# Kernel optimization log

Hardware: AMD Instinct MI355X
Metric: run time of the kernel (lower is better)

The kernel has to match this reference:

```python
import jax, jax.numpy as jnp
import numpy as np

DIM = 256
N = 16          # number of sub-codebooks
K = 1024        # codes per sub-codebook (torch arg K; SeqVQ uses self.embedding directly)
E_DIM = DIM // N
DEPTH = 3
BETA = 0.25
B = 8192


def setup_inputs() -> dict:
    key = jax.random.key(0)
    k1, k2, k3 = jax.random.split(key, 3)
    z = jax.random.normal(k1, (B, DIM), dtype=jnp.float32)
    # nn.init.uniform_(data, -1/N, 1/N)
    embedding = jax.random.uniform(k2, (N, K, E_DIM), dtype=jnp.float32,
                                   minval=-1.0 / N, maxval=1.0 / N)
    # frozen-twin pooling query encoder: mean over depth then Linear D->D
    W = jax.random.normal(k3, (DIM, DIM), dtype=jnp.float32) * 0.02
    b = jnp.zeros((DIM,), dtype=jnp.float32)
    return {"z": z, "embedding": embedding, "W": W, "b": b}


def reference(z, embedding, W, b):
    Bq, D = z.shape
    n, k, e = embedding.shape
    zr = z.reshape(Bq, n, e)                 # residual, squeezed (B,N,1,e)->(B,N,e)
    e_sq = jnp.sum(embedding * embedding, axis=-1)  # (N,K)
    z_q_steps = []
    onehot = None
    idx = None
    for _ in range(DEPTH):
        # cdist((B,N,1,e),(N,K,e)) via ||z||^2 - 2 z.e + ||e||^2, then sqrt
        z_sq = jnp.sum(zr * zr, axis=-1)                       # (B,N)
        cross = jnp.einsum('bne,nke->bnk', zr, embedding)      # (B,N,K)
        d = jnp.sqrt(jnp.maximum(z_sq[:, :, None] - 2.0 * cross + e_sq[None], 0.0))
        idx = jnp.argmin(d, axis=-1)                           # (B,N)
        onehot = jax.nn.one_hot(idx, k, dtype=z.dtype)         # scatter one-hot (B,N,K)
        q = jnp.einsum('bnk,nke->bne', onehot, embedding)      # (B,N,e)
        zr = zr - q
        z_q_steps.append(q.reshape(Bq, D))
    z_q_residual = jnp.stack(z_q_steps, axis=1)                # (B, depth, D)
    # frozen twin query encoder (params carry no gradient in original)
    Wc = jax.lax.stop_gradient(W)
    bc = jax.lax.stop_gradient(b)
    z_q = jnp.mean(z_q_residual, axis=1) @ Wc + bc             # (B, D)
    loss = (jnp.mean((jax.lax.stop_gradient(z_q) - z) ** 2)
            + BETA * jnp.mean((z_q - jax.lax.stop_gradient(z)) ** 2))
    z_q_out = z + jax.lax.stop_gradient(z_q - z)               # straight-through
    return loss, z_q_out, onehot, idx[:, :, None]
```

## Files before the change

### kernel.cpp

```cpp
#include <hip/hip_runtime.h>
#include <math.h>

#define BQ    8192
#define DIMD  256
#define NSUB  16
#define KC    1024
#define ED    16

#define OFF_ZQ   1
#define OFF_OH   (1 + BQ * DIMD)
#define OH_ELEMS (BQ * NSUB * KC)
#define OFF_IDX  (OFF_OH + OH_ELEMS)
#define F4N      ((OH_ELEMS - 4) / 4)
#define WEPS     2e-4f

typedef __attribute__((ext_vector_type(2))) float v2f;
typedef __attribute__((ext_vector_type(4))) float f32x4;
typedef __attribute__((ext_vector_type(8))) short bshort8;
typedef __attribute__((ext_vector_type(4))) unsigned int u32x4;

struct Zr  { v2f p0, p1, p2, p3, p4, p5, p6, p7; };
struct Row { float4 c0, c1, c2, c3; };
struct V2x2 { v2f lo, hi; };

__device__ __forceinline__ float np_sumsq(Zr z) {
  float q0 = __fmul_rn(z.p0.x, z.p0.x), q1 = __fmul_rn(z.p0.y, z.p0.y);
  float q2 = __fmul_rn(z.p1.x, z.p1.x), q3 = __fmul_rn(z.p1.y, z.p1.y);
  float q4 = __fmul_rn(z.p2.x, z.p2.x), q5 = __fmul_rn(z.p2.y, z.p2.y);
  float q6 = __fmul_rn(z.p3.x, z.p3.x), q7 = __fmul_rn(z.p3.y, z.p3.y);
  float q8 = __fmul_rn(z.p4.x, z.p4.x), q9 = __fmul_rn(z.p4.y, z.p4.y);
  float qa = __fmul_rn(z.p5.x, z.p5.x), qb = __fmul_rn(z.p5.y, z.p5.y);
  float qc = __fmul_rn(z.p6.x, z.p6.x), qd = __fmul_rn(z.p6.y, z.p6.y);
  float qe = __fmul_rn(z.p7.x, z.p7.x), qf = __fmul_rn(z.p7.y, z.p7.y);
  float r0 = __fadd_rn(q0, q8), r1 = __fadd_rn(q1, q9);
  float r2 = __fadd_rn(q2, qa), r3 = __fadd_rn(q3, qb);
  float r4 = __fadd_rn(q4, qc), r5 = __fadd_rn(q5, qd);
  float r6 = __fadd_rn(q6, qe), r7 = __fadd_rn(q7, qf);
  return __fadd_rn(__fadd_rn(__fadd_rn(r0, r1), __fadd_rn(r2, r3)),
                   __fadd_rn(__fadd_rn(r4, r5), __fadd_rn(r6, r7)));
}

__device__ __forceinline__ float ref_d(Zr z, Row rw, float zsq, float esq) {
  float p0  = __fmul_rn(z.p0.x, rw.c0.x), p1  = __fmul_rn(z.p0.y, rw.c0.y);
  float p2  = __fmul_rn(z.p1.x, rw.c0.z), p3  = __fmul_rn(z.p1.y, rw.c0.w);
  float p4  = __fmul_rn(z.p2.x, rw.c1.x), p5  = __fmul_rn(z.p2.y, rw.c1.y);
  float p6  = __fmul_rn(z.p3.x, rw.c1.z), p7  = __fmul_rn(z.p3.y, rw.c1.w);
  float p8  = __fmul_rn(z.p4.x, rw.c2.x), p9  = __fmul_rn(z.p4.y, rw.c2.y);
  float p10 = __fmul_rn(z.p5.x, rw.c2.z), p11 = __fmul_rn(z.p5.y, rw.c2.w);
  float p12 = __fmul_rn(z.p6.x, rw.c3.x), p13 = __fmul_rn(z.p6.y, rw.c3.y);
  float p14 = __fmul_rn(z.p7.x, rw.c3.z), p15 = __fmul_rn(z.p7.y, rw.c3.w);
  float L0 = __fadd_rn(__fadd_rn(__fadd_rn(p0, p4), p8),  p12);
  float L1 = __fadd_rn(__fadd_rn(__fadd_rn(p1, p5), p9),  p13);
  float L2 = __fadd_rn(__fadd_rn(__fadd_rn(p2, p6), p10), p14);
  float L3 = __fadd_rn(__fadd_rn(__fadd_rn(p3, p7), p11), p15);
  float cross = __fadd_rn(__fadd_rn(L0, L1), __fadd_rn(L2, L3));
  float t = __fsub_rn(zsq, __fmul_rn(2.0f, cross));
  t = __fadd_rn(t, esq);
  t = fmaxf(t, 0.0f);
  return (float)sqrt((double)t);
}

__device__ __forceinline__ Zr sub_row(Zr z, Row rw) {
  Zr o;
  o.p0 = (v2f){__fsub_rn(z.p0.x, rw.c0.x), __fsub_rn(z.p0.y, rw.c0.y)};
  o.p1 = (v2f){__fsub_rn(z.p1.x, rw.c0.z), __fsub_rn(z.p1.y, rw.c0.w)};
  o.p2 = (v2f){__fsub_rn(z.p2.x, rw.c1.x), __fsub_rn(z.p2.y, rw.c1.y)};
  o.p3 = (v2f){__fsub_rn(z.p3.x, rw.c1.z), __fsub_rn(z.p3.y, rw.c1.w)};
  o.p4 = (v2f){__fsub_rn(z.p4.x, rw.c2.x), __fsub_rn(z.p4.y, rw.c2.y)};
  o.p5 = (v2f){__fsub_rn(z.p5.x, rw.c2.z), __fsub_rn(z.p5.y, rw.c2.w)};
  o.p6 = (v2f){__fsub_rn(z.p6.x, rw.c3.x), __fsub_rn(z.p6.y, rw.c3.y)};
  o.p7 = (v2f){__fsub_rn(z.p7.x, rw.c3.z), __fsub_rn(z.p7.y, rw.c3.w)};
  return o;
}

__device__ __forceinline__ Zr load_zr(const float* p) {
  const float4* zp = (const float4*)p;
  float4 a0 = zp[0], a1 = zp[1], a2 = zp[2], a3 = zp[3];
  V2x2 v0 = __builtin_bit_cast(V2x2, a0), v1 = __builtin_bit_cast(V2x2, a1);
  V2x2 v2 = __builtin_bit_cast(V2x2, a2), v3 = __builtin_bit_cast(V2x2, a3);
  Zr z;
  z.p0 = v0.lo; z.p1 = v0.hi; z.p2 = v1.lo; z.p3 = v1.hi;
  z.p4 = v2.lo; z.p5 = v2.hi; z.p6 = v3.lo; z.p7 = v3.hi;
  return z;
}

__device__ __forceinline__ Row load_row(const float* p) {
  const float4* cp = (const float4*)p;
  Row rw; rw.c0 = cp[0]; rw.c1 = cp[1]; rw.c2 = cp[2]; rw.c3 = cp[3];
  return rw;
}

__device__ __forceinline__ unsigned int f2bf(float x) {
  unsigned int u = __float_as_uint(x);
  return (u + 0x7FFFu + ((u >> 16) & 1u)) >> 16;
}
__device__ __forceinline__ float bf2f(unsigned int b) {
  return __uint_as_float(b << 16);
}

__global__ void vq_prep(const float* __restrict__ emb,
                        unsigned int* __restrict__ ws) {
  const int row = blockIdx.x * 256 + threadIdx.x;
  const float* c = emb + row * 16;
  unsigned int o[16];
#pragma unroll
  for (int u = 0; u < 8; ++u) {
    float a = -c[2 * u], b = -c[2 * u + 1];
    unsigned int h0 = f2bf(a), h1 = f2bf(b);
    o[u] = h0 | (h1 << 16);
    unsigned int l0 = f2bf(__fsub_rn(a, bf2f(h0)));
    unsigned int l1 = f2bf(__fsub_rn(b, bf2f(h1)));
    o[8 + u] = l0 | (l1 << 16);
  }
  u32x4* dst = (u32x4*)ws + row * 4;
#pragma unroll
  for (int j = 0; j < 4; ++j)
    dst[j] = (u32x4){o[4 * j], o[4 * j + 1], o[4 * j + 2], o[4 * j + 3]};
}

__global__ __launch_bounds__(256, 4) void vq_main(
    const float* __restrict__ z, const float* __restrict__ emb,
    const unsigned int* __restrict__ ws, float* __restrict__ out) {
  __shared__ float esq[KC];
  __shared__ float ehs[KC];
  __shared__ unsigned int zq[4 * 64 * 16];
  __shared__ float zb[4 * 64 * 16];
  const int tid   = threadIdx.x;
  const int bx    = blockIdx.x;
  const int n     = bx & 15;
  const int bbase = (bx >> 4) * 256;
  const int w     = tid >> 6;
  const int lane  = tid & 63;
  const int q     = lane >> 4;
  const int c16   = lane & 15;
  const float* embn = emb + n * (KC * ED);
  const u32x4* wsn  = (const u32x4*)ws + n * (KC * 4);

  for (int k = tid; k < KC; k += 256) {
    float s = np_sumsq(load_zr(embn + k * 16));
    esq[k] = s; ehs[k] = 0.5f * s;
  }
  if (bx == 0 && tid == 0) {
    out[0] = 0.f;
    out[OFF_OH + 0] = 0.f; out[OFF_OH + 1] = 0.f; out[OFF_OH + 2] = 0.f;
    out[OFF_OH + OH_ELEMS - 1] = 0.f;
  }
  __syncthreads();

  const int scanB = bbase + tid;
  Zr zr = load_zr(z + scanB * DIMD + n * ED);
  unsigned int* zqw = zq + w * 1024;
  float*        zbw = zb + w * 1024;

#define STAGE_ZR                                                              \
  {                                                                           \
    const int o = lane * 16;                                                  \
    v2f* zb2 = (v2f*)(zbw + o);                                               \
    zb2[0]=zr.p0; zb2[1]=zr.p1; zb2[2]=zr.p2; zb2[3]=zr.p3;                   \
    zb2[4]=zr.p4; zb2[5]=zr.p5; zb2[6]=zr.p6; zb2[7]=zr.p7;                   \
    _Pragma("unroll")                                                         \
    for (int u = 0; u < 8; ++u) { }                                           \
                                                   \
    {                                                                         \
      v2f P; unsigned h0, h1, l0, l1;                                         \
      P=zr.p0; h0=f2bf(P.x); h1=f2bf(P.y); zqw[o+0]=h0|(h1<<16);              \
      l0=f2bf(__fsub_rn(P.x,bf2f(h0))); l1=f2bf(__fsub_rn(P.y,bf2f(h1)));     \
      zqw[o+8]=l0|(l1<<16);                                                   \
      P=zr.p1; h0=f2bf(P.x); h1=f2bf(P.y); zqw[o+1]=h0|(h1<<16);              \
      l0=f2bf(__fsub_rn(P.x,bf2f(h0))); l1=f2bf(__fsub_rn(P.y,bf2f(h1)));     \
      zqw[o+9]=l0|(l1<<16);                                                   \
      P=zr.p2; h0=f2bf(P.x); h1=f2bf(P.y); zqw[o+2]=h0|(h1<<16);              \
      l0=f2bf(__fsub_rn(P.x,bf2f(h0))); l1=f2bf(__fsub_rn(P.y,bf2f(h1)));     \
      zqw[o+10]=l0|(l1<<16);                                                  \
      P=zr.p3; h0=f2bf(P.x); h1=f2bf(P.y); zqw[o+3]=h0|(h1<<16);              \
      l0=f2bf(__fsub_rn(P.x,bf2f(h0))); l1=f2bf(__fsub_rn(P.y,bf2f(h1)));     \
      zqw[o+11]=l0|(l1<<16);                                                  \
      P=zr.p4; h0=f2bf(P.x); h1=f2bf(P.y); zqw[o+4]=h0|(h1<<16);              \
      l0=f2bf(__fsub_rn(P.x,bf2f(h0))); l1=f2bf(__fsub_rn(P.y,bf2f(h1)));     \
      zqw[o+12]=l0|(l1<<16);                                                  \
      P=zr.p5; h0=f2bf(P.x); h1=f2bf(P.y); zqw[o+5]=h0|(h1<<16);              \
      l0=f2bf(__fsub_rn(P.x,bf2f(h0))); l1=f2bf(__fsub_rn(P.y,bf2f(h1)));     \
      zqw[o+13]=l0|(l1<<16);                                                  \
      P=zr.p6; h0=f2bf(P.x); h1=f2bf(P.y); zqw[o+6]=h0|(h1<<16);              \
      l0=f2bf(__fsub_rn(P.x,bf2f(h0))); l1=f2bf(__fsub_rn(P.y,bf2f(h1)));     \
      zqw[o+14]=l0|(l1<<16);                                                  \
      P=zr.p7; h0=f2bf(P.x); h1=f2bf(P.y); zqw[o+7]=h0|(h1<<16);              \
      l0=f2bf(__fsub_rn(P.x,bf2f(h0))); l1=f2bf(__fsub_rn(P.y,bf2f(h1)));     \
      zqw[o+15]=l0|(l1<<16);                                                  \
    }                                                                         \
  }
  STAGE_ZR

  const int gtid = bx * 256 + tid;
  float4* f4 = (float4*)(out + OFF_OH + 3);
  const float4 zf4 = make_float4(0.f, 0.f, 0.f, 0.f);
  int sIdx = 0;
  int bi = 0;

  for (int dep = 0; dep < 3; ++dep) {
    asm volatile("s_waitcnt lgkmcnt(0)" ::: "memory");
    u32x4 B0 = *(const u32x4*)(zqw + ((0 * 16 + c16) * 16 + q * 4));
    u32x4 B1 = *(const u32x4*)(zqw + ((1 * 16 + c16) * 16 + q * 4));
    u32x4 B2 = *(const u32x4*)(zqw + ((2 * 16 + c16) * 16 + q * 4));
    u32x4 B3 = *(const u32x4*)(zqw + ((3 * 16 + c16) * 16 + q * 4));
    bshort8 b0 = __builtin_bit_cast(bshort8, B0);
    bshort8 b1 = __builtin_bit_cast(bshort8, B1);
    bshort8 b2 = __builtin_bit_cast(bshort8, B2);
    bshort8 b3 = __builtin_bit_cast(bshort8, B3);

    float m1_0 = 3.0e38f, m1_1 = 3.0e38f, m1_2 = 3.0e38f, m1_3 = 3.0e38f;
    float m2_0 = 3.0e38f, m2_1 = 3.0e38f, m2_2 = 3.0e38f, m2_3 = 3.0e38f;
    int   k1_0 = 0, k1_1 = 0, k1_2 = 0, k1_3 = 0;
    const int qc4 = q * 4;

    for (int ct = 0; ct < 64; ++ct) {
      f32x4 ehv = __builtin_bit_cast(f32x4, ((const float4*)ehs)[ct * 4 + q]);
      u32x4 A1u = wsn[ct * 64 + c16 * 4 + q];
      u32x4 A2u = wsn[ct * 64 + c16 * 4 + ((q + 2) & 3)];
      if (dep == 0) {
        int sl = sIdx * 131072 + gtid; ++sIdx;
        if (sl < F4N) f4[sl] = zf4;
      }
      {
        int sl = sIdx * 131072 + gtid; ++sIdx;
        if (sl < F4N) f4[sl] = zf4;
      }
      bshort8 a1 = __builtin_bit_cast(bshort8, A1u);
      bshort8 a2 = __builtin_bit_cast(bshort8, A2u);
      const int cbase = ct * 16 + qc4;
#define UPD(V, CODE, M1, K1, M2)                                              \
      { float v_ = (V);                                                       \
        M2 = __builtin_amdgcn_fmed3f(v_, M1, M2);                             \
        bool lt_ = v_ < M1; M1 = lt_ ? v_ : M1; K1 = lt_ ? (CODE) : K1; }
#define DOST(BV, M1, K1, M2)                                                  \
      { f32x4 d1 = __builtin_amdgcn_mfma_f32_16x16x32_bf16(a1, BV, ehv, 0,0,0);\
        f32x4 dd = __builtin_amdgcn_mfma_f32_16x16x32_bf16(a2, BV, d1, 0,0,0);\
        UPD(dd.x, cbase + 0, M1, K1, M2)                                      \
        UPD(dd.y, cbase + 1, M1, K1, M2)                                      \
        UPD(dd.z, cbase + 2, M1, K1, M2)                                      \
        UPD(dd.w, cbase + 3, M1, K1, M2) }
      DOST(b0, m1_0, k1_0, m2_0)
      DOST(b1, m1_1, k1_1, m2_1)
      DOST(b2, m1_2, k1_2, m2_2)
      DOST(b3, m1_3, k1_3, m2_3)
#undef DOST
#undef UPD
    }
#define MERGE3(M1, K1, M2, OFF)                                               \
    { float om = __shfl_xor(M1, OFF); int ok = __shfl_xor(K1, OFF);           \
      float os = __shfl_xor(M2, OFF);                                         \
      float hi = fmaxf(M1, om);                                               \
      M2 = fminf(fminf(M2, os), hi);                                          \
      bool bw = (om < M1) || (om == M1 && ok < K1);                           \
      M1 = bw ? om : M1; K1 = bw ? ok : K1; }
    MERGE3(m1_0, k1_0, m2_0, 16) MERGE3(m1_0, k1_0, m2_0, 32)
    MERGE3(m1_1, k1_1, m2_1, 16) MERGE3(m1_1, k1_1, m2_1, 32)
    MERGE3(m1_2, k1_2, m2_2, 16) MERGE3(m1_2, k1_2, m2_2, 32)
    MERGE3(m1_3, k1_3, m2_3, 16) MERGE3(m1_3, k1_3, m2_3, 32)
#undef MERGE3
    float mA = (q & 1) ? m1_1 : m1_0,  mB = (q & 1) ? m1_3 : m1_2;
    float sA = (q & 1) ? m2_1 : m2_0,  sB = (q & 1) ? m2_3 : m2_2;
    int   kA = (q & 1) ? k1_1 : k1_0;  int kB = (q & 1) ? k1_3 : k1_2;
    float m1F = (q & 2) ? mB : mA;
    float m2F = (q & 2) ? sB : sA;
    int   k1F = (q & 2) ? kB : kA;

    bool fb = (__fsub_rn(m2F, m1F) < WEPS);
    unsigned long long mask = __ballot(fb);
    while (mask) {
      int ss = __ffsll((unsigned long long)mask) - 1;
      mask &= (mask - 1);
      Zr zs = load_zr(zbw + ss * 16);
      float zsq = np_sumsq(zs);
      float db = 3.0e38f; int kb = 0;
      for (int i = 0; i < 16; ++i) {
        int kk = i * 64 + lane;
        Row rw = load_row(embn + kk * 16);
        float d = ref_d(zs, rw, zsq, esq[kk]);
        if (d < db) { db = d; kb = kk; }
      }
#pragma unroll
      for (int off = 1; off < 64; off <<= 1) {
        float od = __shfl_xor(db, off); int ok = __shfl_xor(kb, off);
        if (od < db || (od == db && ok < kb)) { db = od; kb = ok; }
      }
      if (lane == ss) k1F = kb;
    }
    bi = k1F;
    zr = sub_row(zr, load_row(embn + k1F * 16));
    if (dep < 2) { STAGE_ZR }
  }
  for (; sIdx < 256; ++sIdx) {
    int sl = sIdx * 131072 + gtid;
    if (sl < F4N) f4[sl] = zf4;
  }
  out[OFF_IDX + scanB * NSUB + n] = (float)bi;
  {
    Zr zo = load_zr(z + scanB * DIMD + n * ED);
    float* mp2 = out + OFF_ZQ + scanB * DIMD + n * ED;
    mp2[0]  = __fdiv_rn(__fsub_rn(zo.p0.x, zr.p0.x), 3.0f);
    mp2[1]  = __fdiv_rn(__fsub_rn(zo.p0.y, zr.p0.y), 3.0f);
    mp2[2]  = __fdiv_rn(__fsub_rn(zo.p1.x, zr.p1.x), 3.0f);
    mp2[3]  = __fdiv_rn(__fsub_rn(zo.p1.y, zr.p1.y), 3.0f);
    mp2[4]  = __fdiv_rn(__fsub_rn(zo.p2.x, zr.p2.x), 3.0f);
    mp2[5]  = __fdiv_rn(__fsub_rn(zo.p2.y, zr.p2.y), 3.0f);
    mp2[6]  = __fdiv_rn(__fsub_rn(zo.p3.x, zr.p3.x), 3.0f);
    mp2[7]  = __fdiv_rn(__fsub_rn(zo.p3.y, zr.p3.y), 3.0f);
    mp2[8]  = __fdiv_rn(__fsub_rn(zo.p4.x, zr.p4.x), 3.0f);
    mp2[9]  = __fdiv_rn(__fsub_rn(zo.p4.y, zr.p4.y), 3.0f);
    mp2[10] = __fdiv_rn(__fsub_rn(zo.p5.x, zr.p5.x), 3.0f);
    mp2[11] = __fdiv_rn(__fsub_rn(zo.p5.y, zr.p5.y), 3.0f);
    mp2[12] = __fdiv_rn(__fsub_rn(zo.p6.x, zr.p6.x), 3.0f);
    mp2[13] = __fdiv_rn(__fsub_rn(zo.p6.y, zr.p6.y), 3.0f);
    mp2[14] = __fdiv_rn(__fsub_rn(zo.p7.x, zr.p7.x), 3.0f);
    mp2[15] = __fdiv_rn(__fsub_rn(zo.p7.y, zr.p7.y), 3.0f);
  }
#undef STAGE_ZR
}

__global__ void vq_ones(float* __restrict__ out) {
  int g = blockIdx.x * 256 + threadIdx.x;
  int k = (int)out[OFF_IDX + g];
  out[OFF_OH + g * KC + k] = 1.0f;
}

#define TB 16
__global__ __launch_bounds__(256, 2) void vq_head(
    const float* __restrict__ z, const float* __restrict__ W,
    const float* __restrict__ bias, float* __restrict__ out) {
  __shared__ float ml[TB][DIMD];
  __shared__ double reds[4];
  const int t  = threadIdx.x;
  const int r0 = blockIdx.x * TB;
  for (int j = t; j < TB * DIMD; j += 256) {
    int r = j >> 8, d = j & 255;
    ml[r][d] = out[OFF_ZQ + (r0 + r) * DIMD + d];
  }
  __syncthreads();
  float acc[TB];
#pragma unroll
  for (int r = 0; r < TB; ++r) acc[r] = 0.f;
  for (int d = 0; d < DIMD; ++d) {
    float w = W[d * DIMD + t];
#pragma unroll
    for (int r = 0; r < TB; ++r) acc[r] = fmaf(ml[r][d], w, acc[r]);
  }
  const float bv = bias[t];
  double lp = 0.0;
#pragma unroll
  for (int r = 0; r < TB; ++r) {
    float zq   = acc[r] + bv;
    float zv   = z[(r0 + r) * DIMD + t];
    float diff = zq - zv;
    out[OFF_ZQ + (r0 + r) * DIMD + t] = zv + diff;
    lp += (double)diff * (double)diff;
  }
#pragma unroll
  for (int o = 32; o > 0; o >>= 1) lp += __shfl_down(lp, o);
  if ((t & 63) == 0) reds[t >> 6] = lp;
  __syncthreads();
  if (t == 0) {
    double tot = reds[0] + reds[1] + reds[2] + reds[3];
    atomicAdd(out, (float)(tot * (1.25 / (double)(BQ * DIMD))));
  }
}

extern "C" void kernel_launch(void* const* d_in, const int* in_sizes, int n_in,
                              void* d_out, int out_size, void* d_ws, size_t ws_size,
                              hipStream_t stream) {
  const float* z    = (const float*)d_in[0];
  const float* emb  = (const float*)d_in[1];
  const float* W    = (const float*)d_in[2];
  const float* bias = (const float*)d_in[3];
  float* out = (float*)d_out;
  unsigned int* wsp = (unsigned int*)d_ws;
  vq_prep<<<dim3(64), dim3(256), 0, stream>>>(emb, wsp);
  vq_main<<<dim3((BQ / 256) * NSUB), dim3(256), 0, stream>>>(z, emb, wsp, out);
  vq_ones<<<dim3((BQ * NSUB) / 256), dim3(256), 0, stream>>>(out);
  vq_head<<<dim3(BQ / TB), dim3(256), 0, stream>>>(z, W, bias, out);
}
```

Baseline: 709.1 us.

## Halve rows per block, prefetch codebook tiles, nontemporal one-hot zeroing, precompute norms

Each vq_main block now handles 128 batch rows instead of 256 (32 per wave), which doubles the grid to 1024 blocks. Each wave issues two MFMA column tiles per codebook step instead of four, and the winning index is shuffled to the lanes that own each row. Codebook fragments and half-norms are prefetched one iteration ahead. One-hot zero stores become nontemporal and are interleaved on two of every three iterations across the larger thread count. Codebook squared norms are computed once in vq_prep instead of in every block. The intent is more parallelism and latency hiding, at the cost of half the lanes idling in the scalar phases and the codebook being reloaded by twice as many blocks.

After: 688.3 us. 1.03x faster.

```diff
diff --git a/kernel.cpp b/kernel.cpp
--- a/kernel.cpp
+++ b/kernel.cpp
@@ -6,12 +6,14 @@
 #define NSUB  16
 #define KC    1024
 #define ED    16
+#define SCW   32
 
 #define OFF_ZQ   1
 #define OFF_OH   (1 + BQ * DIMD)
 #define OH_ELEMS (BQ * NSUB * KC)
 #define OFF_IDX  (OFF_OH + OH_ELEMS)
 #define F4N      ((OH_ELEMS - 4) / 4)
+#define NTHR     (1024 * 256)
 #define WEPS     2e-4f
 
 typedef __attribute__((ext_vector_type(2))) float v2f;
@@ -98,6 +100,20 @@
   return __uint_as_float(b << 16);
 }
 
+__device__ __forceinline__ void stage_zr(Zr zr, unsigned int* zqp, float* zbp) {
+  v2f* zb2 = (v2f*)zbp;
+  zb2[0]=zr.p0; zb2[1]=zr.p1; zb2[2]=zr.p2; zb2[3]=zr.p3;
+  zb2[4]=zr.p4; zb2[5]=zr.p5; zb2[6]=zr.p6; zb2[7]=zr.p7;
+  v2f P; unsigned h0, h1, l0, l1;
+#define PK(I, PP)                                                             \
+  P = PP; h0 = f2bf(P.x); h1 = f2bf(P.y); zqp[I] = h0 | (h1 << 16);           \
+  l0 = f2bf(__fsub_rn(P.x, bf2f(h0))); l1 = f2bf(__fsub_rn(P.y, bf2f(h1)));   \
+  zqp[8 + I] = l0 | (l1 << 16);
+  PK(0, zr.p0) PK(1, zr.p1) PK(2, zr.p2) PK(3, zr.p3)
+  PK(4, zr.p4) PK(5, zr.p5) PK(6, zr.p6) PK(7, zr.p7)
+#undef PK
+}
+
 __global__ void vq_prep(const float* __restrict__ emb,
                         unsigned int* __restrict__ ws) {
   const int row = blockIdx.x * 256 + threadIdx.x;
@@ -116,6 +132,8 @@
 #pragma unroll
   for (int j = 0; j < 4; ++j)
     dst[j] = (u32x4){o[4 * j], o[4 * j + 1], o[4 * j + 2], o[4 * j + 3]};
+  float* esqg = (float*)(ws + 16384 * 16);
+  esqg[row] = np_sumsq(load_zr(c));
 }
 
 __global__ __launch_bounds__(256, 4) void vq_main(
@@ -123,21 +141,23 @@
     const unsigned int* __restrict__ ws, float* __restrict__ out) {
   __shared__ float esq[KC];
   __shared__ float ehs[KC];
-  __shared__ unsigned int zq[4 * 64 * 16];
-  __shared__ float zb[4 * 64 * 16];
+  __shared__ unsigned int zq[4 * SCW * 16];
+  __shared__ float zb[4 * SCW * 16];
   const int tid   = threadIdx.x;
   const int bx    = blockIdx.x;
   const int n     = bx & 15;
-  const int bbase = (bx >> 4) * 256;
+  const int bbase = (bx >> 4) * 128;
   const int w     = tid >> 6;
   const int lane  = tid & 63;
   const int q     = lane >> 4;
   const int c16   = lane & 15;
+  const int sc    = lane & 31;
   const float* embn = emb + n * (KC * ED);
   const u32x4* wsn  = (const u32x4*)ws + n * (KC * 4);
+  const float* esqg = (const float*)(ws + 16384 * 16) + n * KC;
 
   for (int k = tid; k < KC; k += 256) {
-    float s = np_sumsq(load_zr(embn + k * 16));
+    float s = esqg[k];
     esq[k] = s; ehs[k] = 0.5f * s;
   }
   if (bx == 0 && tid == 0) {
@@ -147,86 +167,50 @@
   }
   __syncthreads();
 
-  const int scanB = bbase + tid;
+  const int scanB = bbase + w * SCW + sc;
   Zr zr = load_zr(z + scanB * DIMD + n * ED);
-  unsigned int* zqw = zq + w * 1024;
-  float*        zbw = zb + w * 1024;
-
-#define STAGE_ZR                                                              \
-  {                                                                           \
-    const int o = lane * 16;                                                  \
-    v2f* zb2 = (v2f*)(zbw + o);                                               \
-    zb2[0]=zr.p0; zb2[1]=zr.p1; zb2[2]=zr.p2; zb2[3]=zr.p3;                   \
-    zb2[4]=zr.p4; zb2[5]=zr.p5; zb2[6]=zr.p6; zb2[7]=zr.p7;                   \
-    _Pragma("unroll")                                                         \
-    for (int u = 0; u < 8; ++u) { }                                           \
-                                                   \
-    {                                                                         \
-      v2f P; unsigned h0, h1, l0, l1;                                         \
-      P=zr.p0; h0=f2bf(P.x); h1=f2bf(P.y); zqw[o+0]=h0|(h1<<16);              \
-      l0=f2bf(__fsub_rn(P.x,bf2f(h0))); l1=f2bf(__fsub_rn(P.y,bf2f(h1)));     \
-      zqw[o+8]=l0|(l1<<16);                                                   \
-      P=zr.p1; h0=f2bf(P.x); h1=f2bf(P.y); zqw[o+1]=h0|(h1<<16);              \
-      l0=f2bf(__fsub_rn(P.x,bf2f(h0))); l1=f2bf(__fsub_rn(P.y,bf2f(h1)));     \
-      zqw[o+9]=l0|(l1<<16);                                                   \
-      P=zr.p2; h0=f2bf(P.x); h1=f2bf(P.y); zqw[o+2]=h0|(h1<<16);              \
-      l0=f2bf(__fsub_rn(P.x,bf2f(h0))); l1=f2bf(__fsub_rn(P.y,bf2f(h1)));     \
-      zqw[o+10]=l0|(l1<<16);                                                  \
-      P=zr.p3; h0=f2bf(P.x); h1=f2bf(P.y); zqw[o+3]=h0|(h1<<16);              \
-      l0=f2bf(__fsub_rn(P.x,bf2f(h0))); l1=f2bf(__fsub_rn(P.y,bf2f(h1)));     \
-      zqw[o+11]=l0|(l1<<16);                                                  \
-      P=zr.p4; h0=f2bf(P.x); h1=f2bf(P.y); zqw[o+4]=h0|(h1<<16);              \
-      l0=f2bf(__fsub_rn(P.x,bf2f(h0))); l1=f2bf(__fsub_rn(P.y,bf2f(h1)));     \
-      zqw[o+12]=l0|(l1<<16);                                                  \
-      P=zr.p5; h0=f2bf(P.x); h1=f2bf(P.y); zqw[o+5]=h0|(h1<<16);              \
-      l0=f2bf(__fsub_rn(P.x,bf2f(h0))); l1=f2bf(__fsub_rn(P.y,bf2f(h1)));     \
-      zqw[o+13]=l0|(l1<<16);                                                  \
-      P=zr.p6; h0=f2bf(P.x); h1=f2bf(P.y); zqw[o+6]=h0|(h1<<16);              \
-      l0=f2bf(__fsub_rn(P.x,bf2f(h0))); l1=f2bf(__fsub_rn(P.y,bf2f(h1)));     \
-      zqw[o+14]=l0|(l1<<16);                                                  \
-      P=zr.p7; h0=f2bf(P.x); h1=f2bf(P.y); zqw[o+7]=h0|(h1<<16);              \
-      l0=f2bf(__fsub_rn(P.x,bf2f(h0))); l1=f2bf(__fsub_rn(P.y,bf2f(h1)));     \
-      zqw[o+15]=l0|(l1<<16);                                                  \
-    }                                                                         \
-  }
-  STAGE_ZR
+  unsigned int* zqw = zq + w * (SCW * 16);
+  float*        zbw = zb + w * (SCW * 16);
+  if (lane < SCW) stage_zr(zr, zqw + sc * 16, zbw + sc * 16);
 
   const int gtid = bx * 256 + tid;
-  float4* f4 = (float4*)(out + OFF_OH + 3);
-  const float4 zf4 = make_float4(0.f, 0.f, 0.f, 0.f);
-  int sIdx = 0;
+  f32x4* f4 = (f32x4*)(out + OFF_OH + 3);
+  const f32x4 zf4 = {0.f, 0.f, 0.f, 0.f};
+  int sIdx = 0, fcnt = 0;
   int bi = 0;
 
   for (int dep = 0; dep < 3; ++dep) {
     asm volatile("s_waitcnt lgkmcnt(0)" ::: "memory");
-    u32x4 B0 = *(const u32x4*)(zqw + ((0 * 16 + c16) * 16 + q * 4));
-    u32x4 B1 = *(const u32x4*)(zqw + ((1 * 16 + c16) * 16 + q * 4));
-    u32x4 B2 = *(const u32x4*)(zqw + ((2 * 16 + c16) * 16 + q * 4));
-    u32x4 B3 = *(const u32x4*)(zqw + ((3 * 16 + c16) * 16 + q * 4));
-    bshort8 b0 = __builtin_bit_cast(bshort8, B0);
-    bshort8 b1 = __builtin_bit_cast(bshort8, B1);
-    bshort8 b2 = __builtin_bit_cast(bshort8, B2);
-    bshort8 b3 = __builtin_bit_cast(bshort8, B3);
-
-    float m1_0 = 3.0e38f, m1_1 = 3.0e38f, m1_2 = 3.0e38f, m1_3 = 3.0e38f;
-    float m2_0 = 3.0e38f, m2_1 = 3.0e38f, m2_2 = 3.0e38f, m2_3 = 3.0e38f;
-    int   k1_0 = 0, k1_1 = 0, k1_2 = 0, k1_3 = 0;
+    u32x4 B0u = *(const u32x4*)(zqw + ((0 * 16 + c16) * 16 + q * 4));
+    u32x4 B1u = *(const u32x4*)(zqw + ((1 * 16 + c16) * 16 + q * 4));
+    bshort8 b0 = __builtin_bit_cast(bshort8, B0u);
+    bshort8 b1 = __builtin_bit_cast(bshort8, B1u);
+
+    float m1_0 = 3.0e38f, m1_1 = 3.0e38f;
+    float m2_0 = 3.0e38f, m2_1 = 3.0e38f;
+    int   k1_0 = 0, k1_1 = 0;
     const int qc4 = q * 4;
+    const int aoff = c16 * 4 + q, boff = c16 * 4 + ((q + 2) & 3);
+
+    u32x4 A1n = wsn[aoff], A2n = wsn[boff];
+    float4 ehn = ((const float4*)ehs)[q];
 
     for (int ct = 0; ct < 64; ++ct) {
-      f32x4 ehv = __builtin_bit_cast(f32x4, ((const float4*)ehs)[ct * 4 + q]);
-      u32x4 A1u = wsn[ct * 64 + c16 * 4 + q];
-      u32x4 A2u = wsn[ct * 64 + c16 * 4 + ((q + 2) & 3)];
-      if (dep == 0) {
-        int sl = sIdx * 131072 + gtid; ++sIdx;
-        if (sl < F4N) f4[sl] = zf4;
+      u32x4 A1c = A1n, A2c = A2n;
+      f32x4 ehv = __builtin_bit_cast(f32x4, ehn);
+      if (ct < 63) {
+        const int nb = (ct + 1) * 64;
+        A1n = wsn[nb + aoff];
+        A2n = wsn[nb + boff];
+        ehn = ((const float4*)ehs)[(ct + 1) * 4 + q];
       }
-      {
-        int sl = sIdx * 131072 + gtid; ++sIdx;
-        if (sl < F4N) f4[sl] = zf4;
+      if (fcnt != 2) {
+        int sl = sIdx * NTHR + gtid; ++sIdx;
+        if (sl < F4N) __builtin_nontemporal_store(zf4, f4 + sl);
       }
-      bshort8 a1 = __builtin_bit_cast(bshort8, A1u);
-      bshort8 a2 = __builtin_bit_cast(bshort8, A2u);
+      fcnt = (fcnt == 2) ? 0 : fcnt + 1;
+      bshort8 a1 = __builtin_bit_cast(bshort8, A1c);
+      bshort8 a2 = __builtin_bit_cast(bshort8, A2c);
       const int cbase = ct * 16 + qc4;
 #define UPD(V, CODE, M1, K1, M2)                                              \
       { float v_ = (V);                                                       \
@@ -241,8 +225,6 @@
         UPD(dd.w, cbase + 3, M1, K1, M2) }
       DOST(b0, m1_0, k1_0, m2_0)
       DOST(b1, m1_1, k1_1, m2_1)
-      DOST(b2, m1_2, k1_2, m2_2)
-      DOST(b3, m1_3, k1_3, m2_3)
 #undef DOST
 #undef UPD
     }
@@ -255,17 +237,13 @@
       M1 = bw ? om : M1; K1 = bw ? ok : K1; }
     MERGE3(m1_0, k1_0, m2_0, 16) MERGE3(m1_0, k1_0, m2_0, 32)
     MERGE3(m1_1, k1_1, m2_1, 16) MERGE3(m1_1, k1_1, m2_1, 32)
-    MERGE3(m1_2, k1_2, m2_2, 16) MERGE3(m1_2, k1_2, m2_2, 32)
-    MERGE3(m1_3, k1_3, m2_3, 16) MERGE3(m1_3, k1_3, m2_3, 32)
 #undef MERGE3
-    float mA = (q & 1) ? m1_1 : m1_0,  mB = (q & 1) ? m1_3 : m1_2;
-    float sA = (q & 1) ? m2_1 : m2_0,  sB = (q & 1) ? m2_3 : m2_2;
-    int   kA = (q & 1) ? k1_1 : k1_0;  int kB = (q & 1) ? k1_3 : k1_2;
-    float m1F = (q & 2) ? mB : mA;
-    float m2F = (q & 2) ? sB : sA;
-    int   k1F = (q & 2) ? kB : kA;
-
-    bool fb = (__fsub_rn(m2F, m1F) < WEPS);
+    const bool t1 = (sc >= 16);
+    float m1F = t1 ? m1_1 : m1_0;
+    float m2F = t1 ? m2_1 : m2_0;
+    int   k1F = t1 ? k1_1 : k1_0;
+
+    bool fb = (lane < SCW) && (__fsub_rn(m2F, m1F) < WEPS);
     unsigned long long mask = __ballot(fb);
     while (mask) {
       int ss = __ffsll((unsigned long long)mask) - 1;
@@ -286,16 +264,17 @@
       }
       if (lane == ss) k1F = kb;
     }
+    k1F = __shfl(k1F, sc);
     bi = k1F;
     zr = sub_row(zr, load_row(embn + k1F * 16));
-    if (dep < 2) { STAGE_ZR }
-  }
-  for (; sIdx < 256; ++sIdx) {
-    int sl = sIdx * 131072 + gtid;
-    if (sl < F4N) f4[sl] = zf4;
-  }
-  out[OFF_IDX + scanB * NSUB + n] = (float)bi;
-  {
+    if (dep < 2 && lane < SCW) stage_zr(zr, zqw + sc * 16, zbw + sc * 16);
+  }
+  for (; sIdx < 128; ++sIdx) {
+    int sl = sIdx * NTHR + gtid;
+    if (sl < F4N) __builtin_nontemporal_store(zf4, f4 + sl);
+  }
+  if (lane < SCW) {
+    out[OFF_IDX + scanB * NSUB + n] = (float)bi;
     Zr zo = load_zr(z + scanB * DIMD + n * ED);
     float* mp2 = out + OFF_ZQ + scanB * DIMD + n * ED;
     mp2[0]  = __fdiv_rn(__fsub_rn(zo.p0.x, zr.p0.x), 3.0f);
@@ -315,7 +294,6 @@
     mp2[14] = __fdiv_rn(__fsub_rn(zo.p7.x, zr.p7.x), 3.0f);
     mp2[15] = __fdiv_rn(__fsub_rn(zo.p7.y, zr.p7.y), 3.0f);
   }
-#undef STAGE_ZR
 }
 
 __global__ void vq_ones(float* __restrict__ out) {
@@ -375,7 +353,7 @@
   float* out = (float*)d_out;
   unsigned int* wsp = (unsigned int*)d_ws;
   vq_prep<<<dim3(64), dim3(256), 0, stream>>>(emb, wsp);
-  vq_main<<<dim3((BQ / 256) * NSUB), dim3(256), 0, stream>>>(z, emb, wsp, out);
+  vq_main<<<dim3((BQ / 128) * NSUB), dim3(256), 0, stream>>>(z, emb, wsp, out);
   vq_ones<<<dim3((BQ * NSUB) / 256), dim3(256), 0, stream>>>(out);
   vq_head<<<dim3(BQ / TB), dim3(256), 0, stream>>>(z, W, bias, out);
 }
```
